# Performance work log

Measured on AMD Instinct MI355X. Metric: run time of the kernel, lower is better.

Reference implementation:

```python
import jax, jax.numpy as jnp
import numpy as np

FEATURE_DIM = 512
ACTION_DIM = 32
N_EXPERTS = 4
D_HIDDEN = 256
BATCH = 131072


def setup_inputs() -> dict:
    key = jax.random.key(0)
    ks = jax.random.split(key, 7)
    s_in = 1.0 / np.sqrt(FEATURE_DIM)
    s_h = 1.0 / np.sqrt(D_HIDDEN)
    return {
        "features": jax.random.normal(ks[0], (BATCH, FEATURE_DIM), dtype=jnp.float32),
        # gating network: feature_dim -> n_experts
        "Wg": jax.random.normal(ks[1], (FEATURE_DIM, N_EXPERTS), dtype=jnp.float32) * s_in,
        "bg": jnp.zeros((N_EXPERTS,), dtype=jnp.float32),
        # per-expert 2-layer MLP: feature_dim -> d_hidden -> action_dim
        "W1": jax.random.normal(ks[2], (N_EXPERTS, FEATURE_DIM, D_HIDDEN), dtype=jnp.float32) * s_in,
        "b1": jnp.zeros((N_EXPERTS, D_HIDDEN), dtype=jnp.float32),
        "W2": jax.random.normal(ks[3], (N_EXPERTS, D_HIDDEN, ACTION_DIM), dtype=jnp.float32) * s_h,
        "b2": jnp.zeros((N_EXPERTS, ACTION_DIM), dtype=jnp.float32),
    }


def reference(features, Wg, bg, W1, b1, W2, b2):
    # gate: softmax over experts, shape [b, e]
    gate = jax.nn.softmax(features @ Wg + bg, axis=-1)
    # expert MLPs (dense MoE: every expert sees every token)
    h = jax.nn.relu(jnp.einsum("bf,efh->beh", features, W1) + b1)  # [b, e, h]
    expert_out = jnp.einsum("beh,eha->bea", h, W2) + b2            # [b, e, a]
    # gate-weighted mixture -> action mean [b, a]
    action_mean = jnp.einsum("bea,be->ba", expert_out, gate)
    return action_mean
```

## Files before the change

### kernel.cpp

```cpp
#include <hip/hip_runtime.h>
#include <hip/hip_bf16.h>
#include <math.h>

#define FDIM 512
#define NEXP 4
#define HDIM 256
#define ADIM 32
#define BM   128
#define NTHR 512

typedef __attribute__((ext_vector_type(8))) short frag8;
typedef __attribute__((ext_vector_type(4))) float f32x4;

#define W1T_OFF 0
#define W2T_OFF (4*256*512)
#define WGT_OFF (W2T_OFF + 4*32*256)

__device__ inline ushort f2bf(float x) {
    union { float f; unsigned u; } v; v.f = x;
    unsigned r = v.u + 0x7FFFu + ((v.u >> 16) & 1u);
    return (ushort)(r >> 16);
}

__device__ inline frag8 pack8(f32x4 a, f32x4 b) {
    frag8 r;
    r[0] = (short)f2bf(a[0]); r[1] = (short)f2bf(a[1]);
    r[2] = (short)f2bf(a[2]); r[3] = (short)f2bf(a[3]);
    r[4] = (short)f2bf(b[0]); r[5] = (short)f2bf(b[1]);
    r[6] = (short)f2bf(b[2]); r[7] = (short)f2bf(b[3]);
    return r;
}

__device__ __forceinline__ void gl16(const void* g, void* l) {
    __builtin_amdgcn_global_load_lds(
        (const __attribute__((address_space(1))) unsigned int*)g,
        (__attribute__((address_space(3))) unsigned int*)l, 16, 0, 0);
}

__global__ __launch_bounds__(256) void moe_prep(const float* __restrict__ Wg,
                                                const float* __restrict__ W1,
                                                const float* __restrict__ W2,
                                                ushort* __restrict__ ws) {
    const int b = blockIdx.x, t = threadIdx.x;
    if (b < 64) {
        #pragma unroll
        for (int it = 0; it < 4; ++it) {
            int oct = (b * 256 + t) + it * 16384;
            int n = oct & 255, k8 = (oct >> 8) & 63, e = oct >> 14;
            f32x4 v0, v1;
            #pragma unroll
            for (int j = 0; j < 4; ++j) v0[j] = W1[(e*512 + k8*8 + j)*256 + n];
            #pragma unroll
            for (int j = 0; j < 4; ++j) v1[j] = W1[(e*512 + k8*8 + 4 + j)*256 + n];
            *(frag8*)(ws + W1T_OFF + (e*HDIM + n)*FDIM + k8*8) = pack8(v0, v1);
        }
    } else if (b < 80) {
        int oct = (b - 64) * 256 + t;
        int a = oct & 31, n8 = (oct >> 5) & 31, e = oct >> 10;
        f32x4 v0, v1;
        #pragma unroll
        for (int j = 0; j < 4; ++j) v0[j] = W2[(e*HDIM + n8*8 + j)*ADIM + a];
        #pragma unroll
        for (int j = 0; j < 4; ++j) v1[j] = W2[(e*HDIM + n8*8 + 4 + j)*ADIM + a];
        *(frag8*)(ws + W2T_OFF + (e*ADIM + a)*HDIM + n8*8) = pack8(v0, v1);
    } else {
        int oct = (b - 80) * 256 + t;
        int k8 = oct & 63, c = oct >> 6;
        f32x4 v0 = {0,0,0,0}, v1 = {0,0,0,0};
        if (c < NEXP) {
            #pragma unroll
            for (int j = 0; j < 4; ++j) v0[j] = Wg[(k8*8 + j)*NEXP + c];
            #pragma unroll
            for (int j = 0; j < 4; ++j) v1[j] = Wg[(k8*8 + 4 + j)*NEXP + c];
        }
        *(frag8*)(ws + WGT_OFF + c*FDIM + k8*8) = pack8(v0, v1);
    }
}

__global__ __launch_bounds__(NTHR, 2) void moe_main(
        const float* __restrict__ feat, const float* __restrict__ bg,
        const float* __restrict__ b1,  const float* __restrict__ b2,
        const ushort* __restrict__ ws, float* __restrict__ out) {
    __shared__ __attribute__((aligned(16))) unsigned char smem[149504];
    unsigned char* buf0 = smem;
    unsigned char* buf1 = smem + 32768;
    unsigned char* w2b  = smem + 65536;
    unsigned char* hbuf = smem + 81920;
    float*         wgate = (float*)(smem + 147456);

    const int tid = threadIdx.x;
    const int lane = tid & 63;
    const int wave = tid >> 6;
    const int l15 = lane & 15;
    const int lg  = lane >> 4;
    const int row0 = blockIdx.x * BM;
    const int wrow = row0 + wave * 16;
    const char* w1b = (const char*)(ws + W1T_OFF);
    const char* w2g = (const char*)(ws + W2T_OFF);
    const char* wgb = (const char*)(ws + WGT_OFF);

    int thrOff[4], w2Off[2], gOff[2];
    #pragma unroll
    for (int j = 0; j < 4; ++j) {
        int slot = j * 512 + tid, cl = slot >> 4;
        thrOff[j] = cl * 1024 + (((slot & 15) * 16) ^ ((cl & 7) << 4));
    }
    #pragma unroll
    for (int j = 0; j < 2; ++j) {
        int slot = j * 512 + tid, c2 = slot >> 5;
        w2Off[j] = c2 * 512 + (((slot & 31) * 16) ^ ((c2 & 7) << 4));
        int cg = slot >> 6;
        gOff[j] = cg * 1024 + (((slot & 63) * 16) ^ ((cg & 7) << 4));
    }

    #pragma unroll
    for (int j = 0; j < 2; ++j) gl16(wgb + gOff[j], buf1 + j * 8192 + wave * 1024);
    #pragma unroll
    for (int j = 0; j < 4; ++j) gl16(w1b + thrOff[j], buf0 + j * 8192 + wave * 1024);

    frag8 afrag[16];
    {
        const float* fp = feat + (size_t)(wrow + l15) * FDIM + lg * 8;
        #pragma unroll
        for (int g4 = 0; g4 < 4; ++g4) {
            f32x4 t0[4], t1[4];
            #pragma unroll
            for (int s = 0; s < 4; ++s) {
                const float* p = fp + (g4 * 4 + s) * 32;
                t0[s] = *(const f32x4*)p;
                t1[s] = *(const f32x4*)(p + 4);
            }
            #pragma unroll
            for (int s = 0; s < 4; ++s) afrag[g4 * 4 + s] = pack8(t0[s], t1[s]);
        }
    }

    __syncthreads();

    {
        f32x4 ga = {0.f, 0.f, 0.f, 0.f};
        #pragma unroll
        for (int s = 0; s < 16; ++s) {
            frag8 bb = *(const frag8*)(buf1 + l15 * 1024 + ((s * 64 + lg * 16) ^ ((l15 & 7) << 4)));
            ga = __builtin_amdgcn_mfma_f32_16x16x32_bf16(afrag[s], bb, ga, 0, 0, 0);
        }
        float bgv = bg[l15 & 3];
        #pragma unroll
        for (int r = 0; r < 4; ++r) {
            float v = ga[r] + bgv;
            float m = fmaxf(v, __shfl_xor(v, 1));
            m = fmaxf(m, __shfl_xor(m, 2));
            float eV = expf(v - m);
            float sV = eV + __shfl_xor(eV, 1);
            sV += __shfl_xor(sV, 2);
            if (l15 < NEXP) wgate[wave * 64 + (lg * 4 + r) * 4 + l15] = eV / sV;
        }
    }
    __syncthreads();

    f32x4 act[2];
    act[0] = (f32x4){0.f, 0.f, 0.f, 0.f};
    act[1] = (f32x4){0.f, 0.f, 0.f, 0.f};

    for (int e = 0; e < NEXP; ++e) {
        #pragma unroll
        for (int h = 0; h < 2; ++h) {
            f32x4 acc1[8];
            #pragma unroll
            for (int ct = 0; ct < 8; ++ct) acc1[ct] = (f32x4){0.f, 0.f, 0.f, 0.f};

            #pragma unroll
            for (int c = 0; c < 4; ++c) {
                const int g = e * 8 + h * 4 + c;
                if (g < 31) {
                    const int gn = g + 1;
                    const char* sb = w1b + (gn >> 2) * 131072 + (gn & 3) * 256;
                    unsigned char* db = (c & 1) ? buf0 : buf1;
                    #pragma unroll
                    for (int j = 0; j < 4; ++j)
                        gl16(sb + thrOff[j], db + j * 8192 + wave * 1024);
                }
                if (h == 0 && c == 1) {
                    const char* sb2 = w2g + e * 16384;
                    #pragma unroll
                    for (int j = 0; j < 2; ++j)
                        gl16(sb2 + w2Off[j], w2b + j * 8192 + wave * 1024);
                }
                const unsigned char* src = (c & 1) ? buf1 : buf0;
                #pragma unroll
                for (int s = 0; s < 4; ++s) {
                    #pragma unroll
                    for (int ct = 0; ct < 8; ++ct) {
                        frag8 bb = *(const frag8*)(src + (ct * 16 + l15) * 256 +
                                                   ((s * 64 + lg * 16) ^ ((l15 & 7) << 4)));
                        acc1[ct] = __builtin_amdgcn_mfma_f32_16x16x32_bf16(
                            afrag[c * 4 + s], bb, acc1[ct], 0, 0, 0);
                    }
                }
                __syncthreads();
            }

            unsigned char* hb = hbuf + wave * 8192;
            #pragma unroll
            for (int ct = 0; ct < 8; ++ct) {
                int col = h * 128 + ct * 16 + l15;
                float b1v = b1[e * HDIM + col];
                #pragma unroll
                for (int r = 0; r < 4; ++r) {
                    int row = lg * 4 + r;
                    float v = fmaxf(acc1[ct][r] + b1v, 0.f);
                    *(ushort*)(hb + row * 512 + ((col * 2) ^ ((row & 7) << 4))) = f2bf(v);
                }
            }
        }

        asm volatile("s_waitcnt lgkmcnt(0)" ::: "memory");
        __builtin_amdgcn_sched_barrier(0);

        {
            f32x4 acc2[2];
            acc2[0] = (f32x4){0.f, 0.f, 0.f, 0.f};
            acc2[1] = (f32x4){0.f, 0.f, 0.f, 0.f};
            const unsigned char* hb = hbuf + wave * 8192;
            #pragma unroll
            for (int s2 = 0; s2 < 8; ++s2) {
                frag8 ha = *(const frag8*)(hb + l15 * 512 + ((s2 * 64 + lg * 16) ^ ((l15 & 7) << 4)));
                #pragma unroll
                for (int ct2 = 0; ct2 < 2; ++ct2) {
                    frag8 bb = *(const frag8*)(w2b + (ct2 * 16 + l15) * 512 +
                                               ((s2 * 64 + lg * 16) ^ ((l15 & 7) << 4)));
                    acc2[ct2] = __builtin_amdgcn_mfma_f32_16x16x32_bf16(ha, bb, acc2[ct2], 0, 0, 0);
                }
            }
            #pragma unroll
            for (int ct2 = 0; ct2 < 2; ++ct2) {
                float b2v = b2[e * ADIM + ct2 * 16 + l15];
                #pragma unroll
                for (int r = 0; r < 4; ++r) {
                    float gt = wgate[wave * 64 + (lg * 4 + r) * 4 + e];
                    act[ct2][r] += gt * (acc2[ct2][r] + b2v);
                }
            }
        }
    }

    #pragma unroll
    for (int ct2 = 0; ct2 < 2; ++ct2)
        #pragma unroll
        for (int r = 0; r < 4; ++r)
            out[(size_t)(wrow + lg * 4 + r) * ADIM + ct2 * 16 + l15] = act[ct2][r];
}

extern "C" void kernel_launch(void* const* d_in, const int* in_sizes, int n_in,
                              void* d_out, int out_size, void* d_ws, size_t ws_size,
                              hipStream_t stream) {
    const float* feat = (const float*)d_in[0];
    const float* Wg   = (const float*)d_in[1];
    const float* bg   = (const float*)d_in[2];
    const float* W1   = (const float*)d_in[3];
    const float* b1   = (const float*)d_in[4];
    const float* W2   = (const float*)d_in[5];
    const float* b2   = (const float*)d_in[6];
    float* out = (float*)d_out;
    ushort* ws = (ushort*)d_ws;

    moe_prep<<<84, 256, 0, stream>>>(Wg, W1, W2, ws);
    const int nblk = 131072 / BM;
    moe_main<<<nblk, NTHR, 0, stream>>>(feat, bg, b1, b2, ws, out);
}
```

Baseline: 575.0 us.

## Double rows per wave and fold gate weights into hidden activations

Each wave now handles 32 rows (two 16-row tiles), so every W1 fragment read from LDS feeds two MFMAs. This halves weight traffic per row and the number of blocks. The gate weight is multiplied into the ReLU hidden activations, and the second GEMM accumulates across experts in one accumulator, with the gate-weighted b2 bias added at the end. Layer 2 now runs per half of the hidden dimension, which shrinks the hidden buffer. In exchange, register pressure roughly doubles (two A-fragment sets and 16 accumulators), and that may cause spills or lower occupancy under launch_bounds(512,2).

```diff
diff --git a/kernel.cpp b/kernel.cpp
--- a/kernel.cpp
+++ b/kernel.cpp
@@ -6,7 +6,7 @@
 #define NEXP 4
 #define HDIM 256
 #define ADIM 32
-#define BM   128
+#define BM   256
 #define NTHR 512
 
 typedef __attribute__((ext_vector_type(8))) short frag8;
@@ -81,7 +81,7 @@
         const float* __restrict__ feat, const float* __restrict__ bg,
         const float* __restrict__ b1,  const float* __restrict__ b2,
         const ushort* __restrict__ ws, float* __restrict__ out) {
-    __shared__ __attribute__((aligned(16))) unsigned char smem[149504];
+    __shared__ __attribute__((aligned(16))) unsigned char smem[151552];
     unsigned char* buf0 = smem;
     unsigned char* buf1 = smem + 32768;
     unsigned char* w2b  = smem + 65536;
@@ -94,12 +94,12 @@
     const int l15 = lane & 15;
     const int lg  = lane >> 4;
     const int row0 = blockIdx.x * BM;
-    const int wrow = row0 + wave * 16;
+    const int wrow = row0 + wave * 32;
     const char* w1b = (const char*)(ws + W1T_OFF);
     const char* w2g = (const char*)(ws + W2T_OFF);
     const char* wgb = (const char*)(ws + WGT_OFF);
 
-    int thrOff[4], w2Off[2], gOff[2];
+    int thrOff[4], w2Off[2];
     #pragma unroll
     for (int j = 0; j < 4; ++j) {
         int slot = j * 512 + tid, cl = slot >> 4;
@@ -109,18 +109,22 @@
     for (int j = 0; j < 2; ++j) {
         int slot = j * 512 + tid, c2 = slot >> 5;
         w2Off[j] = c2 * 512 + (((slot & 31) * 16) ^ ((c2 & 7) << 4));
-        int cg = slot >> 6;
-        gOff[j] = cg * 1024 + (((slot & 63) * 16) ^ ((cg & 7) << 4));
-    }
-
-    #pragma unroll
-    for (int j = 0; j < 2; ++j) gl16(wgb + gOff[j], buf1 + j * 8192 + wave * 1024);
-    #pragma unroll
-    for (int j = 0; j < 4; ++j) gl16(w1b + thrOff[j], buf0 + j * 8192 + wave * 1024);
-
-    frag8 afrag[16];
-    {
-        const float* fp = feat + (size_t)(wrow + l15) * FDIM + lg * 8;
+    }
+
+    #pragma unroll
+    for (int j = 0; j < 2; ++j) {
+        int slot = j * 512 + tid, cg = slot >> 6;
+        int gO = cg * 1024 + (((slot & 63) * 16) ^ ((cg & 7) << 4));
+        gl16(wgb + gO, buf1 + j * 8192 + wave * 1024);
+    }
+    #pragma unroll
+    for (int j = 0; j < 4; ++j)
+        gl16(w1b + thrOff[j], buf0 + j * 8192 + wave * 1024);
+
+    frag8 afrag[2][16];
+    #pragma unroll
+    for (int rt = 0; rt < 2; ++rt) {
+        const float* fp = feat + (size_t)(wrow + rt * 16 + l15) * FDIM + lg * 8;
         #pragma unroll
         for (int g4 = 0; g4 < 4; ++g4) {
             f32x4 t0[4], t1[4];
@@ -131,43 +135,51 @@
                 t1[s] = *(const f32x4*)(p + 4);
             }
             #pragma unroll
-            for (int s = 0; s < 4; ++s) afrag[g4 * 4 + s] = pack8(t0[s], t1[s]);
+            for (int s = 0; s < 4; ++s) afrag[rt][g4 * 4 + s] = pack8(t0[s], t1[s]);
         }
     }
 
     __syncthreads();
 
     {
-        f32x4 ga = {0.f, 0.f, 0.f, 0.f};
+        f32x4 ga[2];
+        ga[0] = (f32x4){0.f,0.f,0.f,0.f}; ga[1] = (f32x4){0.f,0.f,0.f,0.f};
         #pragma unroll
         for (int s = 0; s < 16; ++s) {
             frag8 bb = *(const frag8*)(buf1 + l15 * 1024 + ((s * 64 + lg * 16) ^ ((l15 & 7) << 4)));
-            ga = __builtin_amdgcn_mfma_f32_16x16x32_bf16(afrag[s], bb, ga, 0, 0, 0);
+            ga[0] = __builtin_amdgcn_mfma_f32_16x16x32_bf16(afrag[0][s], bb, ga[0], 0, 0, 0);
+            ga[1] = __builtin_amdgcn_mfma_f32_16x16x32_bf16(afrag[1][s], bb, ga[1], 0, 0, 0);
         }
         float bgv = bg[l15 & 3];
         #pragma unroll
-        for (int r = 0; r < 4; ++r) {
-            float v = ga[r] + bgv;
-            float m = fmaxf(v, __shfl_xor(v, 1));
-            m = fmaxf(m, __shfl_xor(m, 2));
-            float eV = expf(v - m);
-            float sV = eV + __shfl_xor(eV, 1);
-            sV += __shfl_xor(sV, 2);
-            if (l15 < NEXP) wgate[wave * 64 + (lg * 4 + r) * 4 + l15] = eV / sV;
-        }
+        for (int rt = 0; rt < 2; ++rt)
+            #pragma unroll
+            for (int r = 0; r < 4; ++r) {
+                float v = ga[rt][r] + bgv;
+                float m = fmaxf(v, __shfl_xor(v, 1));
+                m = fmaxf(m, __shfl_xor(m, 2));
+                float eV = expf(v - m);
+                float sV = eV + __shfl_xor(eV, 1);
+                sV += __shfl_xor(sV, 2);
+                if (l15 < NEXP) wgate[(wave * 32 + rt * 16 + lg * 4 + r) * 4 + l15] = eV / sV;
+            }
     }
     __syncthreads();
 
-    f32x4 act[2];
-    act[0] = (f32x4){0.f, 0.f, 0.f, 0.f};
-    act[1] = (f32x4){0.f, 0.f, 0.f, 0.f};
+    f32x4 acc2[2][2];
+    #pragma unroll
+    for (int rt = 0; rt < 2; ++rt)
+        #pragma unroll
+        for (int c2 = 0; c2 < 2; ++c2) acc2[rt][c2] = (f32x4){0.f,0.f,0.f,0.f};
 
     for (int e = 0; e < NEXP; ++e) {
         #pragma unroll
         for (int h = 0; h < 2; ++h) {
-            f32x4 acc1[8];
-            #pragma unroll
-            for (int ct = 0; ct < 8; ++ct) acc1[ct] = (f32x4){0.f, 0.f, 0.f, 0.f};
+            f32x4 acc1[2][8];
+            #pragma unroll
+            for (int rt = 0; rt < 2; ++rt)
+                #pragma unroll
+                for (int ct = 0; ct < 8; ++ct) acc1[rt][ct] = (f32x4){0.f,0.f,0.f,0.f};
 
             #pragma unroll
             for (int c = 0; c < 4; ++c) {
@@ -188,67 +200,69 @@
                 }
                 const unsigned char* src = (c & 1) ? buf1 : buf0;
                 #pragma unroll
-                for (int s = 0; s < 4; ++s) {
+                for (int s = 0; s < 4; ++s)
                     #pragma unroll
                     for (int ct = 0; ct < 8; ++ct) {
                         frag8 bb = *(const frag8*)(src + (ct * 16 + l15) * 256 +
                                                    ((s * 64 + lg * 16) ^ ((l15 & 7) << 4)));
-                        acc1[ct] = __builtin_amdgcn_mfma_f32_16x16x32_bf16(
-                            afrag[c * 4 + s], bb, acc1[ct], 0, 0, 0);
+                        acc1[0][ct] = __builtin_amdgcn_mfma_f32_16x16x32_bf16(
+                            afrag[0][c * 4 + s], bb, acc1[0][ct], 0, 0, 0);
+                        acc1[1][ct] = __builtin_amdgcn_mfma_f32_16x16x32_bf16(
+                            afrag[1][c * 4 + s], bb, acc1[1][ct], 0, 0, 0);
                     }
-                }
                 __syncthreads();
             }
 
             unsigned char* hb = hbuf + wave * 8192;
-            #pragma unroll
-            for (int ct = 0; ct < 8; ++ct) {
-                int col = h * 128 + ct * 16 + l15;
-                float b1v = b1[e * HDIM + col];
+            float b1v[8];
+            #pragma unroll
+            for (int ct = 0; ct < 8; ++ct) b1v[ct] = b1[e * HDIM + h * 128 + ct * 16 + l15];
+            #pragma unroll
+            for (int rt = 0; rt < 2; ++rt)
                 #pragma unroll
                 for (int r = 0; r < 4; ++r) {
-                    int row = lg * 4 + r;
-                    float v = fmaxf(acc1[ct][r] + b1v, 0.f);
-                    *(ushort*)(hb + row * 512 + ((col * 2) ^ ((row & 7) << 4))) = f2bf(v);
-                }
-            }
-        }
-
-        asm volatile("s_waitcnt lgkmcnt(0)" ::: "memory");
-        __builtin_amdgcn_sched_barrier(0);
-
-        {
-            f32x4 acc2[2];
-            acc2[0] = (f32x4){0.f, 0.f, 0.f, 0.f};
-            acc2[1] = (f32x4){0.f, 0.f, 0.f, 0.f};
-            const unsigned char* hb = hbuf + wave * 8192;
-            #pragma unroll
-            for (int s2 = 0; s2 < 8; ++s2) {
-                frag8 ha = *(const frag8*)(hb + l15 * 512 + ((s2 * 64 + lg * 16) ^ ((l15 & 7) << 4)));
+                    int row = rt * 16 + lg * 4 + r;
+                    float gt = wgate[(wave * 32 + row) * 4 + e];
+                    #pragma unroll
+                    for (int ct = 0; ct < 8; ++ct) {
+                        float v = fmaxf(acc1[rt][ct][r] + b1v[ct], 0.f) * gt;
+                        *(ushort*)(hb + row * 256 + (((ct * 16 + l15) * 2) ^ ((row & 7) << 4))) = f2bf(v);
+                    }
+                }
+            asm volatile("s_waitcnt lgkmcnt(0)" ::: "memory");
+            __builtin_amdgcn_sched_barrier(0);
+
+            #pragma unroll
+            for (int s2 = 0; s2 < 4; ++s2) {
+                frag8 ha0 = *(const frag8*)(hb + l15 * 256 +
+                                            ((s2 * 64 + lg * 16) ^ ((l15 & 7) << 4)));
+                frag8 ha1 = *(const frag8*)(hb + (16 + l15) * 256 +
+                                            ((s2 * 64 + lg * 16) ^ ((l15 & 7) << 4)));
                 #pragma unroll
                 for (int ct2 = 0; ct2 < 2; ++ct2) {
-                    frag8 bb = *(const frag8*)(w2b + (ct2 * 16 + l15) * 512 +
+                    frag8 bb = *(const frag8*)(w2b + (ct2 * 16 + l15) * 512 + h * 256 +
                                                ((s2 * 64 + lg * 16) ^ ((l15 & 7) << 4)));
-                    acc2[ct2] = __builtin_amdgcn_mfma_f32_16x16x32_bf16(ha, bb, acc2[ct2], 0, 0, 0);
-                }
-            }
-            #pragma unroll
-            for (int ct2 = 0; ct2 < 2; ++ct2) {
-                float b2v = b2[e * ADIM + ct2 * 16 + l15];
-                #pragma unroll
-                for (int r = 0; r < 4; ++r) {
-                    float gt = wgate[wave * 64 + (lg * 4 + r) * 4 + e];
-                    act[ct2][r] += gt * (acc2[ct2][r] + b2v);
-                }
-            }
-        }
-    }
-
-    #pragma unroll
-    for (int ct2 = 0; ct2 < 2; ++ct2)
-        #pragma unroll
-        for (int r = 0; r < 4; ++r)
-            out[(size_t)(wrow + lg * 4 + r) * ADIM + ct2 * 16 + l15] = act[ct2][r];
+                    acc2[0][ct2] = __builtin_amdgcn_mfma_f32_16x16x32_bf16(ha0, bb, acc2[0][ct2], 0, 0, 0);
+                    acc2[1][ct2] = __builtin_amdgcn_mfma_f32_16x16x32_bf16(ha1, bb, acc2[1][ct2], 0, 0, 0);
+                }
+            }
+        }
+    }
+
+    #pragma unroll
+    for (int ct2 = 0; ct2 < 2; ++ct2) {
+        int col = ct2 * 16 + l15;
+        float b2v0 = b2[col], b2v1 = b2[32 + col], b2v2 = b2[64 + col], b2v3 = b2[96 + col];
+        #pragma unroll
+        for (int rt = 0; rt < 2; ++rt)
+            #pragma unroll
+            for (int r = 0; r < 4; ++r) {
+                int rl = wave * 32 + rt * 16 + lg * 4 + r;
+                f32x4 gv = *(const f32x4*)(wgate + rl * 4);
+                float bs = gv[0]*b2v0 + gv[1]*b2v1 + gv[2]*b2v2 + gv[3]*b2v3;
+                out[(size_t)(row0 + rl) * ADIM + col] = acc2[rt][ct2][r] + bs;
+            }
+    }
 }
 
 extern "C" void kernel_launch(void* const* d_in, const int* in_sizes, int n_in,
```

Result: slower. 753.8 us (+31.1%).
